# Performance work log

Measured on AMD Instinct MI355X. Metric: run time of the kernel, lower is better.

Reference implementation:

```python
import jax, jax.numpy as jnp
import numpy as np


def setup_inputs() -> dict:
    key = jax.random.key(0)
    k1, k2 = jax.random.split(key)
    x = jax.random.normal(k1, (32, 112, 112, 128), dtype=jnp.float32)
    # Conv2D kernel: HWIO layout, 7x7, in=2 (mean,max), out=1
    W = jax.random.normal(k2, (7, 7, 2, 1), dtype=jnp.float32) * 0.1
    b = jnp.zeros((1,), dtype=jnp.float32)
    return {"x": x, "W": W, "b": b}


def reference(x, W, b):
    # channel statistics (NHWC, reduce over channel axis)
    mean = jnp.mean(x, axis=-1, keepdims=True)          # [B,H,W,1]
    mx = jnp.max(x, axis=-1, keepdims=True)             # [B,H,W,1]
    merged = jnp.concatenate([mean, mx], axis=-1)       # [B,H,W,2]
    # small 7x7 conv, 'same' padding, 1 output channel
    attn = jax.lax.conv_general_dilated(
        merged, W,
        window_strides=(1, 1),
        padding="SAME",
        dimension_numbers=("NHWC", "HWIO", "NHWC"),
    ) + b                                                 # [B,H,W,1]
    gate = jax.nn.sigmoid(attn)
    return x * gate                                       # broadcast multiply
```

## Files before the change

### kernel.cpp

```cpp
#include <hip/hip_runtime.h>

static constexpr int Bn = 32;
static constexpr int Hn = 112;
static constexpr int Wn = 112;
static constexpr int HALO = 3;
static constexpr int NROWS = Bn * Hn;
static constexpr int SPIN_MAX = 150;

typedef float floatx4 __attribute__((ext_vector_type(4)));

union f2u { float2 f; unsigned long long u; };

__global__ __launch_bounds__(256) void fused_reg_kernel(const float* __restrict__ x,
                                                        const float* __restrict__ Wc,
                                                        const float* __restrict__ bias,
                                                        unsigned long long* __restrict__ stats,
                                                        int* __restrict__ flags,
                                                        float* __restrict__ out) {
    __shared__ float2 sdat[7][Wn + 2 * HALO];
    __shared__ float  glds[Wn];
    __shared__ float  w[98];
    __shared__ int    rowstate[7];

    const int wid  = blockIdx.x;
    const int b    = wid / Hn;
    const int r    = wid % Hn;
    const int tid  = threadIdx.x;
    const int lane = tid & 31;
    const int grp  = tid >> 5;

    const floatx4* __restrict__ x4 = reinterpret_cast<const floatx4*>(x);
    const size_t rowbase = (size_t)wid * Wn * 32;

    float xa[14], xb[14], xc[14], xd[14];
#pragma unroll
    for (int j = 0; j < 14; ++j) {
        const int c = grp + 8 * j;
        const floatx4 v = x4[rowbase + (size_t)c * 32 + lane];
        xa[j] = v.x; xb[j] = v.y; xc[j] = v.z; xd[j] = v.w;
    }

    if (tid < 98) w[tid] = Wc[tid];
    for (int i = tid; i < 7 * (Wn + 2 * HALO); i += 256)
        ((float2*)sdat)[i] = make_float2(0.f, 0.f);
    __syncthreads();

#pragma unroll
    for (int j = 0; j < 14; ++j) {
        const int c = grp + 8 * j;
        float s = xa[j] + xb[j] + xc[j] + xd[j];
        float m = fmaxf(fmaxf(xa[j], xb[j]), fmaxf(xc[j], xd[j]));
#pragma unroll
        for (int off = 16; off >= 1; off >>= 1) {
            s += __shfl_xor(s, off);
            m = fmaxf(m, __shfl_xor(m, off));
        }
        if (lane == 0) {
            f2u t; t.f = make_float2(s * (1.0f / 128.0f), m);
            sdat[HALO][c + HALO] = t.f;
            __hip_atomic_store(&stats[(size_t)wid * Wn + c], t.u,
                               __ATOMIC_RELAXED, __HIP_MEMORY_SCOPE_AGENT);
        }
    }

#pragma unroll
    for (int j = 0; j < 14; ++j)
        asm volatile("" : "+v"(xa[j]), "+v"(xb[j]), "+v"(xc[j]), "+v"(xd[j]));

    asm volatile("s_waitcnt vmcnt(0)" ::: "memory");
    __syncthreads();
    if (tid == 0)
        __hip_atomic_store(&flags[wid], 1, __ATOMIC_RELAXED, __HIP_MEMORY_SCOPE_AGENT);

    if (tid < 7) {
        int st = 0;
        if (tid != HALO) {
            const int rr = r - HALO + tid;
            if (rr < 0 || rr >= Hn) st = 2;
            else {
                const int f = wid - HALO + tid;
                int it = 0, got = 0;
                do {
                    got = __hip_atomic_load(&flags[f], __ATOMIC_RELAXED,
                                            __HIP_MEMORY_SCOPE_AGENT);
                } while (!got && ++it < SPIN_MAX);
                st = got ? 1 : 3;
            }
        }
        rowstate[tid] = st;
    }
    __syncthreads();

    for (int p = tid; p < 7 * Wn; p += 256) {
        const int kr = p / Wn;
        const int c  = p % Wn;
        if (rowstate[kr] == 1) {
            f2u t;
            t.u = __hip_atomic_load(&stats[(size_t)(wid - HALO + kr) * Wn + c],
                                    __ATOMIC_RELAXED, __HIP_MEMORY_SCOPE_AGENT);
            sdat[kr][c + HALO] = t.f;
        }
    }
    for (int kr = 0; kr < 7; ++kr) {
        if (rowstate[kr] != 3) continue;
        const int rr = r - HALO + kr;
        const size_t rb = ((size_t)(b * Hn + rr)) * Wn * 32;
        for (int pc = grp; pc < Wn; pc += 8) {
            const floatx4 v = x4[rb + (size_t)pc * 32 + lane];
            float s = v.x + v.y + v.z + v.w;
            float m = fmaxf(fmaxf(v.x, v.y), fmaxf(v.z, v.w));
#pragma unroll
            for (int off = 16; off >= 1; off >>= 1) {
                s += __shfl_xor(s, off);
                m = fmaxf(m, __shfl_xor(m, off));
            }
            if (lane == 0) sdat[kr][pc + HALO] = make_float2(s * (1.0f / 128.0f), m);
        }
    }
    __syncthreads();

    if (tid < Wn) {
        float acc = bias[0];
#pragma unroll
        for (int kh = 0; kh < 7; ++kh)
#pragma unroll
            for (int kw = 0; kw < 7; ++kw) {
                const float2 sv = sdat[kh][tid + kw];
                acc = fmaf(sv.x, w[(kh * 7 + kw) * 2 + 0], acc);
                acc = fmaf(sv.y, w[(kh * 7 + kw) * 2 + 1], acc);
            }
        glds[tid] = 1.0f / (1.0f + expf(-acc));
    }
    __syncthreads();

    floatx4* __restrict__ o4 = reinterpret_cast<floatx4*>(out);
#pragma unroll
    for (int j = 0; j < 14; ++j) {
        const int c = grp + 8 * j;
        const float g = glds[c];
        floatx4 v;
        v.x = xa[j] * g; v.y = xb[j] * g; v.z = xc[j] * g; v.w = xd[j] * g;
        __builtin_nontemporal_store(v, &o4[rowbase + (size_t)c * 32 + lane]);
    }
}

extern "C" void kernel_launch(void* const* d_in, const int* in_sizes, int n_in,
                              void* d_out, int out_size, void* d_ws, size_t ws_size,
                              hipStream_t stream) {
    const float* x  = (const float*)d_in[0];
    const float* Wc = (const float*)d_in[1];
    const float* bb = (const float*)d_in[2];
    float* out = (float*)d_out;

    unsigned long long* stats = (unsigned long long*)d_ws;
    int* flags = (int*)((char*)d_ws + (size_t)NROWS * Wn * sizeof(unsigned long long));

    hipMemsetAsync(flags, 0, NROWS * sizeof(int), stream);
    fused_reg_kernel<<<NROWS, 256, 0, stream>>>(x, Wc, bb, stats, flags, out);
}
```

Measured before the change: 88.30 us.

## Process two image rows per block to halve halo exchange and block count

Each block now handles a pair of adjacent rows with 512 threads instead of one row with 256. The 7x7 conv reads an 8-row stats window, so only six neighbouring rows have to come through cross-block flags and global stats, and the number of spin-waits and flag checks is halved. The cost is a larger block holding the same per-thread register tile, which may lower occupancy and make the cross-block dependency chains longer. There is also a risk of slower fallback recomputation when neighbouring blocks are not yet resident.

```diff
diff --git a/kernel.cpp b/kernel.cpp
--- a/kernel.cpp
+++ b/kernel.cpp
@@ -4,61 +4,66 @@
 static constexpr int Hn = 112;
 static constexpr int Wn = 112;
 static constexpr int HALO = 3;
-static constexpr int NROWS = Bn * Hn;
+static constexpr int PAIRS_PER_IMG = Hn / 2;
+static constexpr int NPAIR = Bn * PAIRS_PER_IMG;
 static constexpr int SPIN_MAX = 150;
 
 typedef float floatx4 __attribute__((ext_vector_type(4)));
 
 union f2u { float2 f; unsigned long long u; };
 
-__global__ __launch_bounds__(256) void fused_reg_kernel(const float* __restrict__ x,
-                                                        const float* __restrict__ Wc,
-                                                        const float* __restrict__ bias,
-                                                        unsigned long long* __restrict__ stats,
-                                                        int* __restrict__ flags,
-                                                        float* __restrict__ out) {
-    __shared__ float2 sdat[7][Wn + 2 * HALO];
-    __shared__ float  glds[Wn];
+__global__ __launch_bounds__(512) void fused_pair_kernel(const float* __restrict__ x,
+                                                         const float* __restrict__ Wc,
+                                                         const float* __restrict__ bias,
+                                                         unsigned long long* __restrict__ stats,
+                                                         int* __restrict__ flags,
+                                                         float* __restrict__ out) {
+    __shared__ float2 sdat[8][Wn + 2 * HALO];
+    __shared__ float  glds[2][Wn];
     __shared__ float  w[98];
-    __shared__ int    rowstate[7];
+    __shared__ int    rowstate[8];
 
     const int wid  = blockIdx.x;
-    const int b    = wid / Hn;
-    const int r    = wid % Hn;
+    const int b    = wid / PAIRS_PER_IMG;
+    const int s    = wid % PAIRS_PER_IMG;
+    const int r0   = 2 * s;
     const int tid  = threadIdx.x;
     const int lane = tid & 31;
     const int grp  = tid >> 5;
+    const int gRow = grp >> 3;
+    const int gCol = grp & 7;
 
     const floatx4* __restrict__ x4 = reinterpret_cast<const floatx4*>(x);
-    const size_t rowbase = (size_t)wid * Wn * 32;
+    const size_t rowbase = ((size_t)(b * Hn + r0 + gRow)) * Wn * 32;
 
     float xa[14], xb[14], xc[14], xd[14];
 #pragma unroll
     for (int j = 0; j < 14; ++j) {
-        const int c = grp + 8 * j;
+        const int c = gCol + 8 * j;
         const floatx4 v = x4[rowbase + (size_t)c * 32 + lane];
         xa[j] = v.x; xb[j] = v.y; xc[j] = v.z; xd[j] = v.w;
     }
 
     if (tid < 98) w[tid] = Wc[tid];
-    for (int i = tid; i < 7 * (Wn + 2 * HALO); i += 256)
+    for (int i = tid; i < 8 * (Wn + 2 * HALO); i += 512)
         ((float2*)sdat)[i] = make_float2(0.f, 0.f);
     __syncthreads();
 
+    const size_t myStatRow = (size_t)(b * Hn + r0 + gRow) * Wn;
 #pragma unroll
     for (int j = 0; j < 14; ++j) {
-        const int c = grp + 8 * j;
-        float s = xa[j] + xb[j] + xc[j] + xd[j];
-        float m = fmaxf(fmaxf(xa[j], xb[j]), fmaxf(xc[j], xd[j]));
+        const int c = gCol + 8 * j;
+        float sm = xa[j] + xb[j] + xc[j] + xd[j];
+        float mx = fmaxf(fmaxf(xa[j], xb[j]), fmaxf(xc[j], xd[j]));
 #pragma unroll
         for (int off = 16; off >= 1; off >>= 1) {
-            s += __shfl_xor(s, off);
-            m = fmaxf(m, __shfl_xor(m, off));
+            sm += __shfl_xor(sm, off);
+            mx = fmaxf(mx, __shfl_xor(mx, off));
         }
         if (lane == 0) {
-            f2u t; t.f = make_float2(s * (1.0f / 128.0f), m);
-            sdat[HALO][c + HALO] = t.f;
-            __hip_atomic_store(&stats[(size_t)wid * Wn + c], t.u,
+            f2u t; t.f = make_float2(sm * (1.0f / 128.0f), mx);
+            sdat[3 + gRow][c + HALO] = t.f;
+            __hip_atomic_store(&stats[myStatRow + c], t.u,
                                __ATOMIC_RELAXED, __HIP_MEMORY_SCOPE_AGENT);
         }
     }
@@ -72,13 +77,17 @@
     if (tid == 0)
         __hip_atomic_store(&flags[wid], 1, __ATOMIC_RELAXED, __HIP_MEMORY_SCOPE_AGENT);
 
-    if (tid < 7) {
-        int st = 0;
-        if (tid != HALO) {
-            const int rr = r - HALO + tid;
+    if (tid < 8) {
+        const int k = tid;
+        int st;
+        if (k == 3 || k == 4) st = 0;
+        else {
+            const int rr = r0 - HALO + k;
             if (rr < 0 || rr >= Hn) st = 2;
             else {
-                const int f = wid - HALO + tid;
+                const int ps = s + ((k < 3) ? ((k == 0) ? -2 : -1)
+                                            : ((k == 7) ? 2 : 1));
+                const int f = b * PAIRS_PER_IMG + ps;
                 int it = 0, got = 0;
                 do {
                     got = __hip_atomic_load(&flags[f], __ATOMIC_RELAXED,
@@ -87,57 +96,60 @@
                 st = got ? 1 : 3;
             }
         }
-        rowstate[tid] = st;
+        rowstate[k] = st;
     }
     __syncthreads();
 
-    for (int p = tid; p < 7 * Wn; p += 256) {
-        const int kr = p / Wn;
-        const int c  = p % Wn;
-        if (rowstate[kr] == 1) {
+    for (int p = tid; p < 8 * Wn; p += 512) {
+        const int k = p / Wn;
+        const int c = p % Wn;
+        if (rowstate[k] == 1) {
+            const int rr = r0 - HALO + k;
             f2u t;
-            t.u = __hip_atomic_load(&stats[(size_t)(wid - HALO + kr) * Wn + c],
+            t.u = __hip_atomic_load(&stats[(size_t)(b * Hn + rr) * Wn + c],
                                     __ATOMIC_RELAXED, __HIP_MEMORY_SCOPE_AGENT);
-            sdat[kr][c + HALO] = t.f;
+            sdat[k][c + HALO] = t.f;
         }
     }
-    for (int kr = 0; kr < 7; ++kr) {
-        if (rowstate[kr] != 3) continue;
-        const int rr = r - HALO + kr;
+    for (int k = 0; k < 8; ++k) {
+        if (rowstate[k] != 3) continue;
+        const int rr = r0 - HALO + k;
         const size_t rb = ((size_t)(b * Hn + rr)) * Wn * 32;
-        for (int pc = grp; pc < Wn; pc += 8) {
+        for (int pc = grp; pc < Wn; pc += 16) {
             const floatx4 v = x4[rb + (size_t)pc * 32 + lane];
-            float s = v.x + v.y + v.z + v.w;
-            float m = fmaxf(fmaxf(v.x, v.y), fmaxf(v.z, v.w));
+            float sm = v.x + v.y + v.z + v.w;
+            float mx = fmaxf(fmaxf(v.x, v.y), fmaxf(v.z, v.w));
 #pragma unroll
             for (int off = 16; off >= 1; off >>= 1) {
-                s += __shfl_xor(s, off);
-                m = fmaxf(m, __shfl_xor(m, off));
+                sm += __shfl_xor(sm, off);
+                mx = fmaxf(mx, __shfl_xor(mx, off));
             }
-            if (lane == 0) sdat[kr][pc + HALO] = make_float2(s * (1.0f / 128.0f), m);
+            if (lane == 0) sdat[k][pc + HALO] = make_float2(sm * (1.0f / 128.0f), mx);
         }
     }
     __syncthreads();
 
-    if (tid < Wn) {
+    if (tid < 2 * Wn) {
+        const int row = tid / Wn;
+        const int c   = tid % Wn;
         float acc = bias[0];
 #pragma unroll
         for (int kh = 0; kh < 7; ++kh)
 #pragma unroll
             for (int kw = 0; kw < 7; ++kw) {
-                const float2 sv = sdat[kh][tid + kw];
+                const float2 sv = sdat[row + kh][c + kw];
                 acc = fmaf(sv.x, w[(kh * 7 + kw) * 2 + 0], acc);
                 acc = fmaf(sv.y, w[(kh * 7 + kw) * 2 + 1], acc);
             }
-        glds[tid] = 1.0f / (1.0f + expf(-acc));
+        glds[row][c] = 1.0f / (1.0f + expf(-acc));
     }
     __syncthreads();
 
     floatx4* __restrict__ o4 = reinterpret_cast<floatx4*>(out);
 #pragma unroll
     for (int j = 0; j < 14; ++j) {
-        const int c = grp + 8 * j;
-        const float g = glds[c];
+        const int c = gCol + 8 * j;
+        const float g = glds[gRow][c];
         floatx4 v;
         v.x = xa[j] * g; v.y = xb[j] * g; v.z = xc[j] * g; v.w = xd[j] * g;
         __builtin_nontemporal_store(v, &o4[rowbase + (size_t)c * 32 + lane]);
@@ -153,8 +165,8 @@
     float* out = (float*)d_out;
 
     unsigned long long* stats = (unsigned long long*)d_ws;
-    int* flags = (int*)((char*)d_ws + (size_t)NROWS * Wn * sizeof(unsigned long long));
+    int* flags = (int*)((char*)d_ws + (size_t)Bn * Hn * Wn * sizeof(unsigned long long));
 
-    hipMemsetAsync(flags, 0, NROWS * sizeof(int), stream);
-    fused_reg_kernel<<<NROWS, 256, 0, stream>>>(x, Wc, bb, stats, flags, out);
+    hipMemsetAsync(flags, 0, NPAIR * sizeof(int), stream);
+    fused_pair_kernel<<<NPAIR, 512, 0, stream>>>(x, Wc, bb, stats, flags, out);
 }
```

After: 92.81 us. 5.1% more time.
